# Kernel optimization log

Hardware: AMD Instinct MI355X
Metric: run time of the kernel (lower is better)

## Reference

```python
import jax, jax.numpy as jnp
import numpy as np


def setup_inputs() -> dict:
    key = jax.random.key(0)
    ks = jax.random.split(key, 6)
    dim, dt_rank, dim_inner, d_state, channels, batch = 1024, 64, 1024, 128, 64, 8
    rn = lambda k, shape, sc: (jax.random.normal(k, shape, jnp.float32) * sc)
    return {
        "x": rn(ks[0], (batch, channels, dim), 1.0),
        "proj_w": rn(ks[1], (dim, dim), dim ** -0.5),
        "proj_b": jnp.zeros((dim,), jnp.float32),
        "conv_w": rn(ks[2], (channels, channels, 3), (channels * 3) ** -0.5),
        "conv_b": jnp.zeros((channels,), jnp.float32),
        "deltaBC_w": rn(ks[3], (dt_rank + 2 * d_state, dim), dim ** -0.5),
        "dt_proj_w": rn(ks[4], (dim_inner, dt_rank), dt_rank ** -0.5),
        "dt_proj_b": jnp.zeros((dim_inner,), jnp.float32),
        "A_log": jnp.log(jnp.broadcast_to(
            jnp.arange(1, d_state + 1, dtype=jnp.float32), (dim_inner, d_state))),
        "D": jnp.ones((dim_inner,), jnp.float32),
    }


def _silu(x):
    return x * jax.nn.sigmoid(x)


def _selective_scan(x, delta, A, B, C, D):
    # x, delta: (b, l, ed); A: (ed, n); B, C: (b, l, n); D: (ed)
    deltaA = jnp.exp(delta[..., None] * A)                      # (b, l, ed, n)
    BX = delta[..., None] * B[:, :, None, :] * x[..., None]     # (b, l, ed, n)

    def binop(e1, e2):
        a1, b1 = e1
        a2, b2 = e2
        return a1 * a2, a2 * b1 + b2

    # h_t = deltaA_t * h_{t-1} + BX_t  (parallel scan over sequence axis)
    _, hs = jax.lax.associative_scan(binop, (deltaA, BX), axis=1)
    y = jnp.einsum("blen,bln->ble", hs, C) + D * x
    return y


def reference(x, proj_w, proj_b, conv_w, conv_b, deltaBC_w,
              dt_proj_w, dt_proj_b, A_log, D):
    dt_rank = dt_proj_w.shape[1]
    d_state = A_log.shape[1]

    skip = x
    # same self.proj applied to both branches
    x1 = x @ proj_w.T + proj_b
    x2 = x1

    # Conv1d over the feature axis, treating seq positions as channels (L == channels)
    x1 = jax.lax.conv_general_dilated(
        x1, conv_w, window_strides=(1,), padding=[(1, 1)],
        dimension_numbers=("NCH", "OIH", "NCH")) + conv_b[None, :, None]
    x1 = _silu(x1)

    # SSM
    A = -jnp.exp(A_log)
    dbc = x1 @ deltaBC_w.T                                      # (b, l, dt_rank + 2n)
    delta = dbc[..., :dt_rank]
    Bm = dbc[..., dt_rank:dt_rank + d_state]
    Cm = dbc[..., dt_rank + d_state:]
    delta = jax.nn.softplus(delta @ dt_proj_w.T + dt_proj_b)    # (b, l, ed)
    y = _selective_scan(x1, delta, A, Bm, Cm, D)

    out = y * _silu(x2) + skip
    return out @ proj_w.T + proj_b
```

## Files before the change

### kernel.cpp

```cpp
#include <hip/hip_runtime.h>
#include <hip/hip_bf16.h>
#include <math.h>

typedef __hip_bfloat16 bf16;
typedef __attribute__((ext_vector_type(8))) short bf16x8;
typedef __attribute__((ext_vector_type(4))) float f32x4;

#define DIM     1024
#define DT_RANK 64
#define D_STATE 128
#define CHAN    64
#define BATCH   8
#define ROWS    (BATCH*CHAN)
#define DBC_N   (DT_RANK + 2*D_STATE)

#define SZ_X    (ROWS*DIM)
#define SZ_PW   (DIM*DIM)
#define SZ_PB   (DIM)
#define SZ_CW   (CHAN*CHAN*3)
#define SZ_CB   (CHAN)
#define SZ_DBCW (DBC_N*DIM)
#define SZ_DTW  (DIM*DT_RANK)
#define SZ_DTB  (DIM)
#define SZ_ALOG (DIM*D_STATE)
#define SZ_D    (DIM)

#define O0 0
#define O1 (O0+SZ_X)
#define O2 (O1+SZ_PW)
#define O3 (O2+SZ_PB)
#define O4 (O3+SZ_CW)
#define O5 (O4+SZ_CB)
#define O6 (O5+SZ_DBCW)
#define O7 (O6+SZ_DTW)
#define O8 (O7+SZ_DTB)
#define O9 (O8+SZ_ALOG)
#define TOTAL (O9+SZ_D)

__device__ __forceinline__ unsigned short f2b(float v) {
    bf16 t = __float2bfloat16(v);
    return *reinterpret_cast<unsigned short*>(&t);
}

__global__ __launch_bounds__(256) void convert_kernel(
    const void* __restrict__ s0, const void* __restrict__ s1,
    const void* __restrict__ s2, const void* __restrict__ s3,
    const void* __restrict__ s4, const void* __restrict__ s5,
    const void* __restrict__ s6, const void* __restrict__ s7,
    const void* __restrict__ s8, const void* __restrict__ s9,
    float* __restrict__ dstf, bf16* __restrict__ dstb,
    int* __restrict__ flag, const unsigned* __restrict__ dsrc)
{
    const int isb = (dsrc[0] == 0x3F803F80u) ? 1 : 0;
    if (blockIdx.x == 0 && threadIdx.x == 0) *flag = isb;
    int idx = blockIdx.x * 256 + threadIdx.x;
    if (idx >= TOTAL) return;
    const void* src; int base;
    if      (idx < O1) { src = s0; base = O0; }
    else if (idx < O2) { src = s1; base = O1; }
    else if (idx < O3) { src = s2; base = O2; }
    else if (idx < O4) { src = s3; base = O3; }
    else if (idx < O5) { src = s4; base = O4; }
    else if (idx < O6) { src = s5; base = O5; }
    else if (idx < O7) { src = s6; base = O6; }
    else if (idx < O8) { src = s7; base = O7; }
    else if (idx < O9) { src = s8; base = O8; }
    else               { src = s9; base = O9; }
    const int rel = idx - base;
    float v;
    if (isb) v = __bfloat162float(((const bf16*)src)[rel]);
    else     v = ((const float*)src)[rel];
    dstf[idx] = v;
    dstb[idx] = __float2bfloat16(v);
}

template<int ACT, int OUTMODE, int K>
__global__ __launch_bounds__(256) void gemm_mfma(
    const bf16* __restrict__ A, const bf16* __restrict__ B,
    const float* __restrict__ bias, void* __restrict__ C0, bf16* __restrict__ C1,
    int lda, int ldb, int ldc, const int* __restrict__ flagp)
{
    __shared__ float red[4][32][36];
    const int l  = threadIdx.x & 63;
    const int w  = threadIdx.x >> 6;
    const int m0 = blockIdx.y * 32;
    const int n0 = blockIdx.x * 32;
    const int fr = l & 15;
    const int ko = (l >> 4) * 8;

    const bf16* Abase = A + (size_t)(m0 + fr) * lda + ko;
    const bf16* Bbase = B + (size_t)(n0 + fr) * ldb + ko;

    f32x4 acc00 = {}, acc01 = {}, acc10 = {}, acc11 = {};

    #pragma unroll 2
    for (int ks = w; ks * 32 < K; ks += 4) {
        const int k0 = ks * 32;
        bf16x8 a0 = *reinterpret_cast<const bf16x8*>(Abase + k0);
        bf16x8 a1 = *reinterpret_cast<const bf16x8*>(Abase + (size_t)16 * lda + k0);
        bf16x8 b0 = *reinterpret_cast<const bf16x8*>(Bbase + k0);
        bf16x8 b1 = *reinterpret_cast<const bf16x8*>(Bbase + (size_t)16 * ldb + k0);
        acc00 = __builtin_amdgcn_mfma_f32_16x16x32_bf16(a0, b0, acc00, 0, 0, 0);
        acc01 = __builtin_amdgcn_mfma_f32_16x16x32_bf16(a0, b1, acc01, 0, 0, 0);
        acc10 = __builtin_amdgcn_mfma_f32_16x16x32_bf16(a1, b0, acc10, 0, 0, 0);
        acc11 = __builtin_amdgcn_mfma_f32_16x16x32_bf16(a1, b1, acc11, 0, 0, 0);
    }

    {
        const int cr = (l >> 4) * 4;
        const int cc = l & 15;
        #pragma unroll
        for (int v = 0; v < 4; ++v) {
            red[w][cr + v][cc]           = acc00[v];
            red[w][cr + v][16 + cc]      = acc01[v];
            red[w][16 + cr + v][cc]      = acc10[v];
            red[w][16 + cr + v][16 + cc] = acc11[v];
        }
    }
    __syncthreads();

    const int t = threadIdx.x;
    const int r = t >> 3;
    const int c = (t & 7) * 4;
    float o[4];
    #pragma unroll
    for (int q = 0; q < 4; ++q) {
        float s = red[0][r][c + q] + red[1][r][c + q]
                + red[2][r][c + q] + red[3][r][c + q];
        if (bias) s += bias[n0 + c + q];
        if (ACT == 1) s = (s > 20.0f) ? s : log1pf(__expf(s));
        o[q] = s;
    }
    const int m = m0 + r, nn = n0 + c;
    const size_t off = (size_t)m * ldc + nn;
    if (OUTMODE == 0) {
        *reinterpret_cast<float4*>((float*)C0 + off) = make_float4(o[0], o[1], o[2], o[3]);
    } else if (OUTMODE == 2) {
        *reinterpret_cast<float4*>((float*)C0 + off) = make_float4(o[0], o[1], o[2], o[3]);
        ushort4 u; u.x = f2b(o[0]); u.y = f2b(o[1]); u.z = f2b(o[2]); u.w = f2b(o[3]);
        *reinterpret_cast<ushort4*>(C1 + off) = u;
    } else {
        if (*flagp) {
            ushort4 u; u.x = f2b(o[0]); u.y = f2b(o[1]); u.z = f2b(o[2]); u.w = f2b(o[3]);
            *reinterpret_cast<ushort4*>((bf16*)C0 + off) = u;
        } else {
            *reinterpret_cast<float4*>((float*)C0 + off) = make_float4(o[0], o[1], o[2], o[3]);
        }
    }
}

__global__ __launch_bounds__(256) void conv_silu_kernel(
    const float* __restrict__ xin, const float* __restrict__ cw,
    const float* __restrict__ cb, float* __restrict__ xout,
    bf16* __restrict__ xout_bf)
{
    __shared__ float row[DIM + 2];
    const int o   = blockIdx.x;
    const int n   = blockIdx.y;
    const int tid = threadIdx.x;
    const int h0  = tid * 4;
    if (tid == 0) { row[0] = 0.0f; row[DIM + 1] = 0.0f; }
    float acc0 = 0.f, acc1 = 0.f, acc2 = 0.f, acc3 = 0.f;
    for (int i = 0; i < CHAN; ++i) {
        float4 xv = *reinterpret_cast<const float4*>(&xin[(size_t)(n * CHAN + i) * DIM + h0]);
        float w0 = cw[(o * CHAN + i) * 3 + 0];
        float w1 = cw[(o * CHAN + i) * 3 + 1];
        float w2 = cw[(o * CHAN + i) * 3 + 2];
        __syncthreads();
        row[1 + h0] = xv.x; row[2 + h0] = xv.y;
        row[3 + h0] = xv.z; row[4 + h0] = xv.w;
        __syncthreads();
        float r0 = row[h0],     r1 = row[h0 + 1], r2 = row[h0 + 2];
        float r3 = row[h0 + 3], r4 = row[h0 + 4], r5 = row[h0 + 5];
        acc0 = fmaf(r0, w0, fmaf(r1, w1, fmaf(r2, w2, acc0)));
        acc1 = fmaf(r1, w0, fmaf(r2, w1, fmaf(r3, w2, acc1)));
        acc2 = fmaf(r2, w0, fmaf(r3, w1, fmaf(r4, w2, acc2)));
        acc3 = fmaf(r3, w0, fmaf(r4, w1, fmaf(r5, w2, acc3)));
    }
    float bb = cb[o];
    size_t base = (size_t)(n * CHAN + o) * DIM + h0;
    float v0 = acc0 + bb, v1 = acc1 + bb, v2 = acc2 + bb, v3 = acc3 + bb;
    v0 = v0 / (1.0f + __expf(-v0));
    v1 = v1 / (1.0f + __expf(-v1));
    v2 = v2 / (1.0f + __expf(-v2));
    v3 = v3 / (1.0f + __expf(-v3));
    *reinterpret_cast<float4*>(&xout[base]) = make_float4(v0, v1, v2, v3);
    ushort4 u; u.x = f2b(v0); u.y = f2b(v1); u.z = f2b(v2); u.w = f2b(v3);
    *reinterpret_cast<ushort4*>(&xout_bf[base]) = u;
}

__device__ __forceinline__ float quad_sum(float x) {
    int v;
    v = __builtin_amdgcn_update_dpp(0, __float_as_int(x), 0xB1, 0xf, 0xf, true);
    x += __int_as_float(v);
    v = __builtin_amdgcn_update_dpp(0, __float_as_int(x), 0x4E, 0xf, 0xf, true);
    x += __int_as_float(v);
    return x;
}

#define EPW 4
__global__ __launch_bounds__(256) void scan_kernel(
    const float* __restrict__ xskip,
    const float* __restrict__ x2,
    const float* __restrict__ xc,
    const float* __restrict__ dbc,
    const float* __restrict__ delta,
    const float* __restrict__ A_log,
    const float* __restrict__ Dp,
    bf16*        __restrict__ outp)
{
    __shared__ float sDB[4][CHAN][2 * EPW];
    __shared__ float sPart[4][EPW][CHAN][16];
    const int w    = threadIdx.x >> 6;
    const int lane = threadIdx.x & 63;
    const int bb   = blockIdx.x >> 6;
    const int eb   = (blockIdx.x & 63) * (4 * EPW) + w * EPW;
    const int r0   = bb * CHAN;
    const int r    = r0 + lane;

    const float4 dlt4 = *reinterpret_cast<const float4*>(&delta[(size_t)r * DIM + eb]);
    const float4 xv4  = *reinterpret_cast<const float4*>(&xc   [(size_t)r * DIM + eb]);
    const float4 x24  = *reinterpret_cast<const float4*>(&x2   [(size_t)r * DIM + eb]);
    const float4 xs4  = *reinterpret_cast<const float4*>(&xskip[(size_t)r * DIM + eb]);
    const float4 dv4  = *reinterpret_cast<const float4*>(&Dp[eb]);

    const float C_LOG2E = 1.44269504f;
    float a0[EPW], a1[EPW], ga[EPW], fb[EPW];
    const float dl[EPW] = {dlt4.x, dlt4.y, dlt4.z, dlt4.w};
    const float xl[EPW] = {xv4.x,  xv4.y,  xv4.z,  xv4.w};
    const float x2l[EPW]= {x24.x,  x24.y,  x24.z,  x24.w};
    const float xsl[EPW]= {xs4.x,  xs4.y,  xs4.z,  xs4.w};
    const float dvl[EPW]= {dv4.x,  dv4.y,  dv4.z,  dv4.w};
    #pragma unroll
    for (int j = 0; j < EPW; ++j) {
        const float2 al = *reinterpret_cast<const float2*>(
            &A_log[(size_t)(eb + j) * D_STATE + 2 * lane]);
        a0[j] = -__expf(al.x) * C_LOG2E;
        a1[j] = -__expf(al.y) * C_LOG2E;
        ga[j] = x2l[j] / (1.0f + __expf(-x2l[j]));
        fb[j] = fmaf(dvl[j] * xl[j], ga[j], xsl[j]);
    }
    *reinterpret_cast<float4*>(&sDB[w][lane][0]) =
        make_float4(dl[0], dl[0] * xl[0], dl[1], dl[1] * xl[1]);
    *reinterpret_cast<float4*>(&sDB[w][lane][4]) =
        make_float4(dl[2], dl[2] * xl[2], dl[3], dl[3] * xl[3]);
    __syncthreads();

    float h0[EPW] = {}, h1[EPW] = {};
    const float* bp = dbc + (size_t)r0 * DBC_N + DT_RANK + 2 * lane;
    const float* cp = bp + D_STATE;
    float2 bv = *reinterpret_cast<const float2*>(bp);
    float2 cv = *reinterpret_cast<const float2*>(cp);

    #pragma unroll 4
    for (int l = 0; l < CHAN; ++l) {
        const int ln = (l < CHAN - 1) ? (l + 1) : l;
        const float2 bn = *reinterpret_cast<const float2*>(bp + (size_t)ln * DBC_N);
        const float2 cn = *reinterpret_cast<const float2*>(cp + (size_t)ln * DBC_N);

        const float4 d0 = *reinterpret_cast<const float4*>(&sDB[w][l][0]);
        const float4 d1 = *reinterpret_cast<const float4*>(&sDB[w][l][4]);
        const float dltj[EPW]  = {d0.x, d0.z, d1.x, d1.z};
        const float dltxj[EPW] = {d0.y, d0.w, d1.y, d1.w};

        float part[EPW];
        #pragma unroll
        for (int j = 0; j < EPW; ++j) {
            const float e0 = exp2f(dltj[j] * a0[j]);
            const float e1 = exp2f(dltj[j] * a1[j]);
            h0[j] = fmaf(e0, h0[j], dltxj[j] * bv.x);
            h1[j] = fmaf(e1, h1[j], dltxj[j] * bv.y);
            part[j] = quad_sum(fmaf(h0[j], cv.x, h1[j] * cv.y));
        }
        if ((lane & 3) == 0) {
            const int q = lane >> 2;
            sPart[w][0][l][q] = part[0];
            sPart[w][1][l][q] = part[1];
            sPart[w][2][l][q] = part[2];
            sPart[w][3][l][q] = part[3];
        }
        bv = bn; cv = cn;
    }
    __syncthreads();

    ushort4 u;
    unsigned short* up = reinterpret_cast<unsigned short*>(&u);
    #pragma unroll
    for (int j = 0; j < EPW; ++j) {
        const float4 p0 = *reinterpret_cast<const float4*>(&sPart[w][j][lane][0]);
        const float4 p1 = *reinterpret_cast<const float4*>(&sPart[w][j][lane][4]);
        const float4 p2 = *reinterpret_cast<const float4*>(&sPart[w][j][lane][8]);
        const float4 p3 = *reinterpret_cast<const float4*>(&sPart[w][j][lane][12]);
        float y = ((p0.x + p0.y) + (p0.z + p0.w)) + ((p1.x + p1.y) + (p1.z + p1.w))
                + ((p2.x + p2.y) + (p2.z + p2.w)) + ((p3.x + p3.y) + (p3.z + p3.w));
        up[j] = f2b(fmaf(y, ga[j], fb[j]));
    }
    *reinterpret_cast<ushort4*>(&outp[(size_t)r * DIM + eb]) = u;
}

extern "C" void kernel_launch(void* const* d_in, const int* in_sizes, int n_in,
                              void* d_out, int out_size, void* d_ws, size_t ws_size,
                              hipStream_t stream) {
    float* ws   = (float*)d_ws;
    int*   flag = (int*)d_ws;
    float* inF  = ws + 16;
    bf16*  inB  = (bf16*)(inF + TOTAL);

    float* x1_pre = (float*)(inB + TOTAL);
    float* x1c    = x1_pre + (size_t)ROWS * DIM;
    bf16*  x1c_bf = (bf16*)(x1c + (size_t)ROWS * DIM);
    float* dbc    = (float*)(x1c_bf + (size_t)ROWS * DIM);
    bf16*  dbc_bf = (bf16*)(dbc + (size_t)ROWS * DBC_N);
    float* delta  = (float*)(dbc_bf + (size_t)ROWS * DBC_N);
    bf16*  outp_bf= (bf16*)(delta + (size_t)ROWS * DIM);

    convert_kernel<<<(TOTAL + 255) / 256, 256, 0, stream>>>(
        d_in[0], d_in[1], d_in[2], d_in[3], d_in[4],
        d_in[5], d_in[6], d_in[7], d_in[8], d_in[9],
        inF, inB, flag, (const unsigned*)d_in[9]);

    gemm_mfma<0, 0, DIM><<<dim3(DIM / 32, ROWS / 32), 256, 0, stream>>>(
        inB + O0, inB + O1, inF + O2, x1_pre, nullptr, DIM, DIM, DIM, nullptr);
    conv_silu_kernel<<<dim3(CHAN, BATCH), 256, 0, stream>>>(x1_pre, inF + O3, inF + O4, x1c, x1c_bf);
    gemm_mfma<0, 2, DIM><<<dim3(DBC_N / 32, ROWS / 32), 256, 0, stream>>>(
        x1c_bf, inB + O5, nullptr, dbc, dbc_bf, DIM, DIM, DBC_N, nullptr);
    gemm_mfma<1, 0, DT_RANK><<<dim3(DIM / 32, ROWS / 32), 256, 0, stream>>>(
        dbc_bf, inB + O6, inF + O7, delta, nullptr, DBC_N, DT_RANK, DIM, nullptr);
    scan_kernel<<<dim3(BATCH * (DIM / (4 * EPW))), 256, 0, stream>>>(
        inF + O0, x1_pre, x1c, dbc, delta, inF + O8, inF + O9, outp_bf);
    gemm_mfma<0, 1, DIM><<<dim3(DIM / 32, ROWS / 32), 256, 0, stream>>>(
        outp_bf, inB + O1, inF + O2, d_out, nullptr, DIM, DIM, DIM, flag);
}
```

Baseline: 96.99 us.

## Vectorize conversion, drop conv LDS barriers, stage B/C in LDS with full-wave DPP reduction

The input conversion kernel now handles four elements per thread with vector loads and stores. The conv kernel reads its halo neighbours straight from global memory, removing two barriers per channel iteration. The scan kernel stages the B/C rows in shared memory and software-pipelines the reads. It also reduces across all 64 lanes with DPP row and broadcast ops instead of quad sums followed by an LDS reduction. GEMM unroll is raised to 4. The vectorized convert assumes every segment boundary is a multiple of 4, and the 64-lane DPP reduction assumes the row_bcast patterns behave correctly on this architecture.

```diff
diff --git a/kernel.cpp b/kernel.cpp
--- a/kernel.cpp
+++ b/kernel.cpp
@@ -41,6 +41,9 @@
     bf16 t = __float2bfloat16(v);
     return *reinterpret_cast<unsigned short*>(&t);
 }
+__device__ __forceinline__ float b162f(unsigned short s) {
+    return __uint_as_float(((unsigned)s) << 16);
+}
 
 __global__ __launch_bounds__(256) void convert_kernel(
     const void* __restrict__ s0, const void* __restrict__ s1,
@@ -53,7 +56,7 @@
 {
     const int isb = (dsrc[0] == 0x3F803F80u) ? 1 : 0;
     if (blockIdx.x == 0 && threadIdx.x == 0) *flag = isb;
-    int idx = blockIdx.x * 256 + threadIdx.x;
+    int idx = (blockIdx.x * 256 + threadIdx.x) * 4;
     if (idx >= TOTAL) return;
     const void* src; int base;
     if      (idx < O1) { src = s0; base = O0; }
@@ -67,11 +70,16 @@
     else if (idx < O9) { src = s8; base = O8; }
     else               { src = s9; base = O9; }
     const int rel = idx - base;
-    float v;
-    if (isb) v = __bfloat162float(((const bf16*)src)[rel]);
-    else     v = ((const float*)src)[rel];
-    dstf[idx] = v;
-    dstb[idx] = __float2bfloat16(v);
+    float4 v;
+    if (isb) {
+        ushort4 s = *reinterpret_cast<const ushort4*>((const bf16*)src + rel);
+        v.x = b162f(s.x); v.y = b162f(s.y); v.z = b162f(s.z); v.w = b162f(s.w);
+    } else {
+        v = *reinterpret_cast<const float4*>((const float*)src + rel);
+    }
+    *reinterpret_cast<float4*>(&dstf[idx]) = v;
+    ushort4 u; u.x = f2b(v.x); u.y = f2b(v.y); u.z = f2b(v.z); u.w = f2b(v.w);
+    *reinterpret_cast<ushort4*>(&dstb[idx]) = u;
 }
 
 template<int ACT, int OUTMODE, int K>
@@ -93,7 +101,7 @@
 
     f32x4 acc00 = {}, acc01 = {}, acc10 = {}, acc11 = {};
 
-    #pragma unroll 2
+    #pragma unroll 4
     for (int ks = w; ks * 32 < K; ks += 4) {
         const int k0 = ks * 32;
         bf16x8 a0 = *reinterpret_cast<const bf16x8*>(Abase + k0);
@@ -154,30 +162,28 @@
     const float* __restrict__ cb, float* __restrict__ xout,
     bf16* __restrict__ xout_bf)
 {
-    __shared__ float row[DIM + 2];
     const int o   = blockIdx.x;
     const int n   = blockIdx.y;
     const int tid = threadIdx.x;
     const int h0  = tid * 4;
-    if (tid == 0) { row[0] = 0.0f; row[DIM + 1] = 0.0f; }
+    const float* xrow = xin + (size_t)n * CHAN * DIM;
+    const float* wrow = cw + o * CHAN * 3;
     float acc0 = 0.f, acc1 = 0.f, acc2 = 0.f, acc3 = 0.f;
+    #pragma unroll 4
     for (int i = 0; i < CHAN; ++i) {
-        float4 xv = *reinterpret_cast<const float4*>(&xin[(size_t)(n * CHAN + i) * DIM + h0]);
-        float w0 = cw[(o * CHAN + i) * 3 + 0];
-        float w1 = cw[(o * CHAN + i) * 3 + 1];
-        float w2 = cw[(o * CHAN + i) * 3 + 2];
-        __syncthreads();
-        row[1 + h0] = xv.x; row[2 + h0] = xv.y;
-        row[3 + h0] = xv.z; row[4 + h0] = xv.w;
-        __syncthreads();
-        float r0 = row[h0],     r1 = row[h0 + 1], r2 = row[h0 + 2];
-        float r3 = row[h0 + 3], r4 = row[h0 + 4], r5 = row[h0 + 5];
-        acc0 = fmaf(r0, w0, fmaf(r1, w1, fmaf(r2, w2, acc0)));
-        acc1 = fmaf(r1, w0, fmaf(r2, w1, fmaf(r3, w2, acc1)));
-        acc2 = fmaf(r2, w0, fmaf(r3, w1, fmaf(r4, w2, acc2)));
-        acc3 = fmaf(r3, w0, fmaf(r4, w1, fmaf(r5, w2, acc3)));
-    }
-    float bb = cb[o];
+        const float* xr = xrow + (size_t)i * DIM;
+        const float4 xv = *reinterpret_cast<const float4*>(&xr[h0]);
+        const float left  = (h0 > 0)        ? xr[h0 - 1] : 0.0f;
+        const float right = (h0 + 4 < DIM)  ? xr[h0 + 4] : 0.0f;
+        const float w0 = wrow[i * 3 + 0];
+        const float w1 = wrow[i * 3 + 1];
+        const float w2 = wrow[i * 3 + 2];
+        acc0 = fmaf(left, w0, fmaf(xv.x, w1, fmaf(xv.y, w2, acc0)));
+        acc1 = fmaf(xv.x, w0, fmaf(xv.y, w1, fmaf(xv.z, w2, acc1)));
+        acc2 = fmaf(xv.y, w0, fmaf(xv.z, w1, fmaf(xv.w, w2, acc2)));
+        acc3 = fmaf(xv.z, w0, fmaf(xv.w, w1, fmaf(right, w2, acc3)));
+    }
+    const float bb = cb[o];
     size_t base = (size_t)(n * CHAN + o) * DIM + h0;
     float v0 = acc0 + bb, v1 = acc1 + bb, v2 = acc2 + bb, v3 = acc3 + bb;
     v0 = v0 / (1.0f + __expf(-v0));
@@ -189,12 +195,14 @@
     *reinterpret_cast<ushort4*>(&xout_bf[base]) = u;
 }
 
-__device__ __forceinline__ float quad_sum(float x) {
+__device__ __forceinline__ float sum64_dpp(float x) {
     int v;
-    v = __builtin_amdgcn_update_dpp(0, __float_as_int(x), 0xB1, 0xf, 0xf, true);
-    x += __int_as_float(v);
-    v = __builtin_amdgcn_update_dpp(0, __float_as_int(x), 0x4E, 0xf, 0xf, true);
-    x += __int_as_float(v);
+    v = __builtin_amdgcn_update_dpp(0, __float_as_int(x), 0x111, 0xf, 0xf, true); x += __int_as_float(v);
+    v = __builtin_amdgcn_update_dpp(0, __float_as_int(x), 0x112, 0xf, 0xf, true); x += __int_as_float(v);
+    v = __builtin_amdgcn_update_dpp(0, __float_as_int(x), 0x114, 0xf, 0xf, true); x += __int_as_float(v);
+    v = __builtin_amdgcn_update_dpp(0, __float_as_int(x), 0x118, 0xf, 0xf, true); x += __int_as_float(v);
+    v = __builtin_amdgcn_update_dpp(0, __float_as_int(x), 0x142, 0xa, 0xf, true); x += __int_as_float(v);
+    v = __builtin_amdgcn_update_dpp(0, __float_as_int(x), 0x143, 0xc, 0xf, true); x += __int_as_float(v);
     return x;
 }
 
@@ -209,14 +217,26 @@
     const float* __restrict__ Dp,
     bf16*        __restrict__ outp)
 {
-    __shared__ float sDB[4][CHAN][2 * EPW];
-    __shared__ float sPart[4][EPW][CHAN][16];
+    __shared__ float sBC[CHAN][256];
+    __shared__ float sDB[4][CHAN][8];
+    __shared__ float sY[4][CHAN][4];
     const int w    = threadIdx.x >> 6;
     const int lane = threadIdx.x & 63;
     const int bb   = blockIdx.x >> 6;
-    const int eb   = (blockIdx.x & 63) * (4 * EPW) + w * EPW;
+    const int eb   = (blockIdx.x & 63) * 16 + w * 4;
     const int r0   = bb * CHAN;
     const int r    = r0 + lane;
+
+    {
+        const int row = threadIdx.x >> 2;
+        const int c0  = (threadIdx.x & 3) * 64;
+        const float* src = dbc + (size_t)(r0 + row) * DBC_N + DT_RANK + c0;
+        float* dst = &sBC[row][c0];
+        #pragma unroll
+        for (int k = 0; k < 16; ++k)
+            *reinterpret_cast<float4*>(dst + 4 * k) =
+                *reinterpret_cast<const float4*>(src + 4 * k);
+    }
 
     const float4 dlt4 = *reinterpret_cast<const float4*>(&delta[(size_t)r * DIM + eb]);
     const float4 xv4  = *reinterpret_cast<const float4*>(&xc   [(size_t)r * DIM + eb]);
@@ -233,10 +253,8 @@
     const float dvl[EPW]= {dv4.x,  dv4.y,  dv4.z,  dv4.w};
     #pragma unroll
     for (int j = 0; j < EPW; ++j) {
-        const float2 al = *reinterpret_cast<const float2*>(
-            &A_log[(size_t)(eb + j) * D_STATE + 2 * lane]);
-        a0[j] = -__expf(al.x) * C_LOG2E;
-        a1[j] = -__expf(al.y) * C_LOG2E;
+        a0[j] = -__expf(A_log[(size_t)(eb + j) * D_STATE + lane])      * C_LOG2E;
+        a1[j] = -__expf(A_log[(size_t)(eb + j) * D_STATE + 64 + lane]) * C_LOG2E;
         ga[j] = x2l[j] / (1.0f + __expf(-x2l[j]));
         fb[j] = fmaf(dvl[j] * xl[j], ga[j], xsl[j]);
     }
@@ -247,54 +265,44 @@
     __syncthreads();
 
     float h0[EPW] = {}, h1[EPW] = {};
-    const float* bp = dbc + (size_t)r0 * DBC_N + DT_RANK + 2 * lane;
-    const float* cp = bp + D_STATE;
-    float2 bv = *reinterpret_cast<const float2*>(bp);
-    float2 cv = *reinterpret_cast<const float2*>(cp);
+    float4 d0 = *reinterpret_cast<const float4*>(&sDB[w][0][0]);
+    float4 d1 = *reinterpret_cast<const float4*>(&sDB[w][0][4]);
+    float bv0 = sBC[0][lane],       bv1 = sBC[0][64 + lane];
+    float cv0 = sBC[0][128 + lane], cv1 = sBC[0][192 + lane];
 
     #pragma unroll 4
     for (int l = 0; l < CHAN; ++l) {
-        const int ln = (l < CHAN - 1) ? (l + 1) : l;
-        const float2 bn = *reinterpret_cast<const float2*>(bp + (size_t)ln * DBC_N);
-        const float2 cn = *reinterpret_cast<const float2*>(cp + (size_t)ln * DBC_N);
-
-        const float4 d0 = *reinterpret_cast<const float4*>(&sDB[w][l][0]);
-        const float4 d1 = *reinterpret_cast<const float4*>(&sDB[w][l][4]);
+        const int ln = (l + 1) & 63;
+        const float4 d0n = *reinterpret_cast<const float4*>(&sDB[w][ln][0]);
+        const float4 d1n = *reinterpret_cast<const float4*>(&sDB[w][ln][4]);
+        const float bv0n = sBC[ln][lane],       bv1n = sBC[ln][64 + lane];
+        const float cv0n = sBC[ln][128 + lane], cv1n = sBC[ln][192 + lane];
+
         const float dltj[EPW]  = {d0.x, d0.z, d1.x, d1.z};
         const float dltxj[EPW] = {d0.y, d0.w, d1.y, d1.w};
-
         float part[EPW];
         #pragma unroll
         for (int j = 0; j < EPW; ++j) {
             const float e0 = exp2f(dltj[j] * a0[j]);
             const float e1 = exp2f(dltj[j] * a1[j]);
-            h0[j] = fmaf(e0, h0[j], dltxj[j] * bv.x);
-            h1[j] = fmaf(e1, h1[j], dltxj[j] * bv.y);
-            part[j] = quad_sum(fmaf(h0[j], cv.x, h1[j] * cv.y));
+            h0[j] = fmaf(e0, h0[j], dltxj[j] * bv0);
+            h1[j] = fmaf(e1, h1[j], dltxj[j] * bv1);
+            part[j] = sum64_dpp(fmaf(h0[j], cv0, h1[j] * cv1));
         }
-        if ((lane & 3) == 0) {
-            const int q = lane >> 2;
-            sPart[w][0][l][q] = part[0];
-            sPart[w][1][l][q] = part[1];
-            sPart[w][2][l][q] = part[2];
-            sPart[w][3][l][q] = part[3];
-        }
-        bv = bn; cv = cn;
+        if (lane == 63)
+            *reinterpret_cast<float4*>(&sY[w][l][0]) =
+                make_float4(part[0], part[1], part[2], part[3]);
+
+        d0 = d0n; d1 = d1n; bv0 = bv0n; bv1 = bv1n; cv0 = cv0n; cv1 = cv1n;
     }
     __syncthreads();
 
+    const float4 y = *reinterpret_cast<const float4*>(&sY[w][lane][0]);
     ushort4 u;
-    unsigned short* up = reinterpret_cast<unsigned short*>(&u);
-    #pragma unroll
-    for (int j = 0; j < EPW; ++j) {
-        const float4 p0 = *reinterpret_cast<const float4*>(&sPart[w][j][lane][0]);
-        const float4 p1 = *reinterpret_cast<const float4*>(&sPart[w][j][lane][4]);
-        const float4 p2 = *reinterpret_cast<const float4*>(&sPart[w][j][lane][8]);
-        const float4 p3 = *reinterpret_cast<const float4*>(&sPart[w][j][lane][12]);
-        float y = ((p0.x + p0.y) + (p0.z + p0.w)) + ((p1.x + p1.y) + (p1.z + p1.w))
-                + ((p2.x + p2.y) + (p2.z + p2.w)) + ((p3.x + p3.y) + (p3.z + p3.w));
-        up[j] = f2b(fmaf(y, ga[j], fb[j]));
-    }
+    u.x = f2b(fmaf(y.x, ga[0], fb[0]));
+    u.y = f2b(fmaf(y.y, ga[1], fb[1]));
+    u.z = f2b(fmaf(y.z, ga[2], fb[2]));
+    u.w = f2b(fmaf(y.w, ga[3], fb[3]));
     *reinterpret_cast<ushort4*>(&outp[(size_t)r * DIM + eb]) = u;
 }
 
@@ -314,7 +322,7 @@
     float* delta  = (float*)(dbc_bf + (size_t)ROWS * DBC_N);
     bf16*  outp_bf= (bf16*)(delta + (size_t)ROWS * DIM);
 
-    convert_kernel<<<(TOTAL + 255) / 256, 256, 0, stream>>>(
+    convert_kernel<<<(TOTAL / 4 + 255) / 256, 256, 0, stream>>>(
         d_in[0], d_in[1], d_in[2], d_in[3], d_in[4],
         d_in[5], d_in[6], d_in[7], d_in[8], d_in[9],
         inF, inB, flag, (const unsigned*)d_in[9]);
```

Result: slower. 103.5 us (+6.7%).
